# Kernel tuning notes

Hardware: AMD Instinct MI355X
Metric: run time of the kernel (lower is better)

Reference implementation:

```python
import jax, jax.numpy as jnp
import numpy as np

LEVELS = 2
_H0 = jnp.array([0.0322231, -0.01260397, -0.09921954, 0.2978578,
                 0.80373875, 0.49761867, -0.02963553, -0.07576571], dtype=jnp.float32)
_H1 = _H0[::-1] * jnp.array([-1.0, 1.0] * 4, dtype=jnp.float32)  # db4 QMF


def subband_conv2d(x, kernel_2d, stride):
    # depthwise grouped conv: same 2D kernel applied to every channel
    C = x.shape[-1]
    k = jnp.tile(kernel_2d[:, :, None, None], (1, 1, 1, C))  # HWIO with I=1, groups=C
    return jax.lax.conv_general_dilated(
        x, k, window_strides=(stride, stride), padding='SAME',
        dimension_numbers=('NHWC', 'HWIO', 'NHWC'), feature_group_count=C)


def _upsample2d(t):
    B, H, W, C = t.shape
    return jnp.zeros((B, 2 * H, 2 * W, C), t.dtype).at[:, ::2, ::2, :].set(t)


def _local_conv(t, w):
    # per-spatial-position linear map over channels: [B,H,W,I] x [I,O,W,H] -> [B,H,W,O]
    return jnp.einsum('bhwi,iowh->bhwo', t, w)


def setup_inputs() -> dict:
    key = jax.random.key(0)
    ks = jax.random.split(key, 9)
    B, H, W, C, O = 16, 128, 128, 64, 64
    inp = {
        'x': jax.random.normal(ks[0], (B, H, W, C), dtype=jnp.float32),
        'wLL': 0.02 * jax.random.normal(ks[1], (C, O, 32, 32), dtype=jnp.float32),
        'wLH_l0': 0.02 * jax.random.normal(ks[2], (C, O, 64, 64), dtype=jnp.float32),
        'wHL_l0': 0.02 * jax.random.normal(ks[3], (C, O, 64, 64), dtype=jnp.float32),
        'wHH_l0': 0.02 * jax.random.normal(ks[4], (C, O, 64, 64), dtype=jnp.float32),
        'wLH_l1': 0.02 * jax.random.normal(ks[5], (C, O, 32, 32), dtype=jnp.float32),
        'wHL_l1': 0.02 * jax.random.normal(ks[6], (C, O, 32, 32), dtype=jnp.float32),
        'wHH_l1': 0.02 * jax.random.normal(ks[7], (C, O, 32, 32), dtype=jnp.float32),
    }
    return inp


def reference(x, wLL, wLH_l0, wHL_l0, wHH_l0, wLH_l1, wHL_l1, wHH_l1):
    h0, h1 = _H0, _H1
    g0, g1 = h0[::-1], h1[::-1]
    # H=W=128 is divisible by 2**levels, so no symmetric padding is needed.
    res = x
    details = []
    for _ in range(LEVELS):
        cLL = subband_conv2d(res, jnp.outer(h0, h0), 2)
        cLH = subband_conv2d(res, jnp.outer(h0, h1), 2)
        cHL = subband_conv2d(res, jnp.outer(h1, h0), 2)
        cHH = subband_conv2d(res, jnp.outer(h1, h1), 2)
        details.append((cLH, cHL, cHH))
        res = cLL
    yA = _local_conv(res, wLL)  # [B,32,32,O]
    det_w = [(wLH_l0, wHL_l0, wHH_l0), (wLH_l1, wHL_l1, wHH_l1)]
    td = []
    for i in range(LEVELS):
        lh, hl, hh = details[i]
        wlh, whl, whh = det_w[i]
        td.append((_local_conv(lh, wlh), _local_conv(hl, whl), _local_conv(hh, whh)))
    r = yA
    for i in reversed(range(LEVELS)):
        yLH, yHL, yHH = td[i]
        r = (subband_conv2d(_upsample2d(r), jnp.outer(g0, g0), 1)
             + subband_conv2d(_upsample2d(yLH), jnp.outer(g0, g1), 1)
             + subband_conv2d(_upsample2d(yHL), jnp.outer(g1, g0), 1)
             + subband_conv2d(_upsample2d(yHH), jnp.outer(g1, g1), 1))
    return r
```

## Files before the change

### kernel.cpp

```cpp
#include <hip/hip_runtime.h>

__device__ __constant__ float H0[8] = { 0.0322231f, -0.01260397f, -0.09921954f,  0.2978578f,
                                        0.80373875f, 0.49761867f, -0.02963553f, -0.07576571f};
__device__ __constant__ float H1[8] = { 0.07576571f, -0.02963553f, -0.49761867f, 0.80373875f,
                                       -0.2978578f, -0.09921954f,  0.01260397f,  0.0322231f};
__device__ __constant__ float G0[8] = {-0.07576571f, -0.02963553f,  0.49761867f, 0.80373875f,
                                        0.2978578f,  -0.09921954f, -0.01260397f, 0.0322231f};
__device__ __constant__ float G1[8] = { 0.0322231f,   0.01260397f, -0.09921954f, -0.2978578f,
                                        0.80373875f, -0.49761867f, -0.02963553f, 0.07576571f};

template<int HIN>
__global__ __launch_bounds__(256) void fwd_dwt(const float* __restrict__ in,
                                               float* __restrict__ oLL, float* __restrict__ oLH,
                                               float* __restrict__ oHL, float* __restrict__ oHH)
{
    constexpr int OH = HIN / 2;
    constexpr int TQ = OH / 2;
    const int tid = threadIdx.x;
    const int c = tid & 63;
    const int s = blockIdx.x * 4 + (tid >> 6);
    const int j = s % TQ;
    const int i = (s / TQ) % TQ;
    const int b = s / (TQ * TQ);

    float acc[2][2][4];
#pragma unroll
    for (int a = 0; a < 2; ++a)
#pragma unroll
        for (int d = 0; d < 2; ++d)
#pragma unroll
            for (int k = 0; k < 4; ++k) acc[a][d][k] = 0.f;

    const int iw0 = 4 * j - 3;
#pragma unroll
    for (int r = 0; r < 10; ++r) {
        const int ih = 4 * i + r - 3;
        if ((unsigned)ih < (unsigned)HIN) {
            const float* row = in + ((b * HIN + ih) * HIN) * 64 + c;
            float xv[10];
#pragma unroll
            for (int v = 0; v < 10; ++v) {
                const int iw = iw0 + v;
                xv[v] = ((unsigned)iw < (unsigned)HIN) ? row[iw * 64] : 0.f;
            }
            float h00 = 0.f, h01 = 0.f, h10 = 0.f, h11 = 0.f;
#pragma unroll
            for (int v = 0; v < 8; ++v) {
                h00 += H0[v] * xv[v];
                h10 += H1[v] * xv[v];
                h01 += H0[v] * xv[v + 2];
                h11 += H1[v] * xv[v + 2];
            }
#pragma unroll
            for (int ii = 0; ii < 2; ++ii) {
                const int u = r - 2 * ii;
                if (0 <= u && u < 8) {
                    const float a0 = H0[u], a1 = H1[u];
                    acc[ii][0][0] += a0 * h00;
                    acc[ii][0][1] += a0 * h10;
                    acc[ii][0][2] += a1 * h00;
                    acc[ii][0][3] += a1 * h10;
                    acc[ii][1][0] += a0 * h01;
                    acc[ii][1][1] += a0 * h11;
                    acc[ii][1][2] += a1 * h01;
                    acc[ii][1][3] += a1 * h11;
                }
            }
        }
    }

#pragma unroll
    for (int ii = 0; ii < 2; ++ii)
#pragma unroll
        for (int jj = 0; jj < 2; ++jj) {
            const int oh = 2 * i + ii, ow = 2 * j + jj;
            const int oidx = ((b * OH + oh) * OH + ow) * 64 + c;
            oLL[oidx] = acc[ii][jj][0];
            oLH[oidx] = acc[ii][jj][1];
            oHL[oidx] = acc[ii][jj][2];
            oHH[oidx] = acc[ii][jj][3];
        }
}

template<int HD>
__global__ __launch_bounds__(256) void local_conv_lds(
    const float* __restrict__ t0, const float* __restrict__ t1,
    const float* __restrict__ t2, const float* __restrict__ t3,
    const float* __restrict__ w0, const float* __restrict__ w1,
    const float* __restrict__ w2, const float* __restrict__ w3,
    float* __restrict__ o0, float* __restrict__ o1,
    float* __restrict__ o2, float* __restrict__ o3)
{
    constexpr int WH  = HD * HD;
    constexpr int HT  = 16;
    constexpr int RSW = 76;
    constexpr int RSA = 20;

    __shared__ __align__(16) float Wl[4][HT][RSW];
    __shared__ __align__(16) float Al[4][HT][RSA];

    const int z = blockIdx.z;
    const float* tin = (z == 0) ? t0 : (z == 1) ? t1 : (z == 2) ? t2 : t3;
    const float* wgt = (z == 0) ? w0 : (z == 1) ? w1 : (z == 2) ? w2 : w3;
    float*       out = (z == 0) ? o0 : (z == 1) ? o1 : (z == 2) ? o2 : o3;

    const int hbase = blockIdx.x * HT;
    const int w     = blockIdx.y;
    const int tid   = threadIdx.x;

    const int so  = tid >> 2;
    const int sh4 = tid & 3;
    const int sb  = tid >> 4;
    const int sha = tid & 15;

    const int hc = tid & 15;
    const int o4 = tid >> 4;

    const float* wp0 = wgt + (so * WH) + w * HD + hbase + sh4 * 4;
    const float* ap0 = tin + ((sb * HD + hbase + sha) * HD + w) * 64;

    float4 acc[16];
#pragma unroll
    for (int b = 0; b < 16; ++b) acc[b] = make_float4(0.f, 0.f, 0.f, 0.f);

    float4 wv[4], av;
#pragma unroll
    for (int r = 0; r < 4; ++r)
        wv[r] = *(const float4*)(wp0 + (size_t)(r * 64) * WH);
    av = *(const float4*)(ap0);

    for (int chunk = 0; chunk < 16; ++chunk) {
        __syncthreads();
#pragma unroll
        for (int r = 0; r < 4; ++r) {
            Wl[r][sh4 * 4 + 0][so] = wv[r].x;
            Wl[r][sh4 * 4 + 1][so] = wv[r].y;
            Wl[r][sh4 * 4 + 2][so] = wv[r].z;
            Wl[r][sh4 * 4 + 3][so] = wv[r].w;
        }
        Al[0][sha][sb] = av.x;
        Al[1][sha][sb] = av.y;
        Al[2][sha][sb] = av.z;
        Al[3][sha][sb] = av.w;
        __syncthreads();

        if (chunk < 15) {
            const int i0n = (chunk + 1) * 4;
#pragma unroll
            for (int r = 0; r < 4; ++r)
                wv[r] = *(const float4*)(wp0 + (size_t)((i0n + r) * 64) * WH);
            av = *(const float4*)(ap0 + i0n);
        }

#pragma unroll
        for (int ii = 0; ii < 4; ++ii) {
            const float4 wf = *(const float4*)&Wl[ii][hc][o4 * 4];
#pragma unroll
            for (int bq = 0; bq < 4; ++bq) {
                const float4 af = *(const float4*)&Al[ii][hc][bq * 4];
                const float* afp = (const float*)&af;
#pragma unroll
                for (int k = 0; k < 4; ++k) {
                    const float a = afp[k];
                    acc[bq * 4 + k].x += a * wf.x;
                    acc[bq * 4 + k].y += a * wf.y;
                    acc[bq * 4 + k].z += a * wf.z;
                    acc[bq * 4 + k].w += a * wf.w;
                }
            }
        }
    }

#pragma unroll
    for (int b = 0; b < 16; ++b)
        *(float4*)(out + ((b * HD + hbase + hc) * HD + w) * 64 + o4 * 4) = acc[b];
}

template<int HOUT>
__global__ __launch_bounds__(256) void inv_dwt(const float* __restrict__ yLL,
                                               const float* __restrict__ yLH,
                                               const float* __restrict__ yHL,
                                               const float* __restrict__ yHH,
                                               float* __restrict__ out)
{
    constexpr int HS = HOUT / 2;
    const int tid = threadIdx.x;
    const int c = tid & 63;
    const int s = blockIdx.x * 4 + (tid >> 6);
    const int j = s % HS;
    const int i = (s / HS) % HS;
    const int b = s / (HS * HS);

    float Pe[4] = {0.f, 0.f, 0.f, 0.f}, Po[4] = {0.f, 0.f, 0.f, 0.f};
    float Qe[4] = {0.f, 0.f, 0.f, 0.f}, Qo[4] = {0.f, 0.f, 0.f, 0.f};

#pragma unroll
    for (int ku = 0; ku < 4; ++ku) {
        const int m = i - 1 + ku;
        if ((unsigned)m < (unsigned)HS) {
            const float a0e = G0[1 + 2 * ku], a0o = G0[2 * ku];
            const float a1e = G1[1 + 2 * ku], a1o = G1[2 * ku];
            const int rowoff = (b * HS + m) * HS;
#pragma unroll
            for (int kv = 0; kv < 4; ++kv) {
                const int n = j - 1 + kv;
                if ((unsigned)n < (unsigned)HS) {
                    const int idx = (rowoff + n) * 64 + c;
                    const float yll = yLL[idx], ylh = yLH[idx];
                    const float yhl = yHL[idx], yhh = yHH[idx];
                    Pe[kv] += a0e * yll + a1e * yhl;
                    Po[kv] += a0o * yll + a1o * yhl;
                    Qe[kv] += a0e * ylh + a1e * yhh;
                    Qo[kv] += a0o * ylh + a1o * yhh;
                }
            }
        }
    }

    float o00 = 0.f, o01 = 0.f, o10 = 0.f, o11 = 0.f;
#pragma unroll
    for (int kv = 0; kv < 4; ++kv) {
        const float b0e = G0[1 + 2 * kv], b0o = G0[2 * kv];
        const float b1e = G1[1 + 2 * kv], b1o = G1[2 * kv];
        o00 += b0e * Pe[kv] + b1e * Qe[kv];
        o01 += b0o * Pe[kv] + b1o * Qe[kv];
        o10 += b0e * Po[kv] + b1e * Qo[kv];
        o11 += b0o * Po[kv] + b1o * Qo[kv];
    }

    const int h0 = 2 * i, w0 = 2 * j;
    const int base = ((b * HOUT + h0) * HOUT + w0) * 64 + c;
    out[base] = o00;
    out[base + 64] = o01;
    out[base + HOUT * 64] = o10;
    out[base + HOUT * 64 + 64] = o11;
}

extern "C" void kernel_launch(void* const* d_in, const int* in_sizes, int n_in,
                              void* d_out, int out_size, void* d_ws, size_t ws_size,
                              hipStream_t stream)
{
    const float* x    = (const float*)d_in[0];
    const float* wLL  = (const float*)d_in[1];
    const float* wLH0 = (const float*)d_in[2];
    const float* wHL0 = (const float*)d_in[3];
    const float* wHH0 = (const float*)d_in[4];
    const float* wLH1 = (const float*)d_in[5];
    const float* wHL1 = (const float*)d_in[6];
    const float* wHH1 = (const float*)d_in[7];
    float* out = (float*)d_out;
    float* ws  = (float*)d_ws;

    const int S0 = 16 * 64 * 64 * 64;
    const int S1 = 16 * 32 * 32 * 64;

    float* c0LL = out;
    float* c0LH = out + 1 * S0;
    float* c0HL = out + 2 * S0;
    float* c0HH = out + 3 * S0;

    float* c1   = ws;
    float* t0   = ws + 4 * S1;
    float* t1   = ws + 4 * S1 + 3 * S0;
    float* yA   = ws + 7 * S1 + 3 * S0;
    float* r1   = ws;

    fwd_dwt<128><<<16 * 32 * 32 / 4, 256, 0, stream>>>(x, c0LL, c0LH, c0HL, c0HH);

    fwd_dwt<64><<<16 * 16 * 16 / 4, 256, 0, stream>>>(c0LL,
        c1 + 0 * S1, c1 + 1 * S1, c1 + 2 * S1, c1 + 3 * S1);

    local_conv_lds<64><<<dim3(4, 64, 3), 256, 0, stream>>>(
        c0LH, c0HL, c0HH, nullptr,
        wLH0, wHL0, wHH0, nullptr,
        t0 + 0 * S0, t0 + 1 * S0, t0 + 2 * S0, nullptr);

    local_conv_lds<32><<<dim3(2, 32, 4), 256, 0, stream>>>(
        c1 + 1 * S1, c1 + 2 * S1, c1 + 3 * S1, c1 + 0 * S1,
        wLH1, wHL1, wHH1, wLL,
        t1 + 0 * S1, t1 + 1 * S1, t1 + 2 * S1, yA);

    inv_dwt<64><<<16 * 32 * 32 / 4, 256, 0, stream>>>(
        yA, t1 + 0 * S1, t1 + 1 * S1, t1 + 2 * S1, r1);

    inv_dwt<128><<<16 * 64 * 64 / 4, 256, 0, stream>>>(
        r1, t0 + 0 * S0, t0 + 1 * S0, t0 + 2 * S0, out);
}
```

Measured before the change: 291.1 us.

## Retile local conv kernel over output-channel groups and 32-wide h tiles

Restructures the per-position channel-mixing kernel so each block covers 32 spatial h positions and a subset of output channels (OT=16 or 8), instead of 16 positions and all 64 outputs. This raises the block count, especially for the 32x32 level, which before launched few blocks relative to the GPU's CU count. The trade-off is that activations are reloaded once per output-channel group and each thread keeps fewer accumulators, so arithmetic per LDS read drops.

```diff
diff --git a/kernel.cpp b/kernel.cpp
--- a/kernel.cpp
+++ b/kernel.cpp
@@ -82,7 +82,7 @@
         }
 }
 
-template<int HD>
+template<int HD, int OT, int HG>
 __global__ __launch_bounds__(256) void local_conv_lds(
     const float* __restrict__ t0, const float* __restrict__ t1,
     const float* __restrict__ t2, const float* __restrict__ t3,
@@ -92,88 +92,115 @@
     float* __restrict__ o2, float* __restrict__ o3)
 {
     constexpr int WH  = HD * HD;
-    constexpr int HT  = 16;
-    constexpr int RSW = 76;
+    constexpr int NQ  = OT / 4;
+    constexpr int BGN = 8 / NQ;
+    constexpr int BG  = 16 / BGN;
+    constexpr int RSW = OT + 4;
     constexpr int RSA = 20;
-
-    __shared__ __align__(16) float Wl[4][HT][RSW];
-    __shared__ __align__(16) float Al[4][HT][RSA];
+    constexpr int WL4 = OT / 8;
+
+    __shared__ __align__(16) float Wl[4][32][RSW];
+    __shared__ __align__(16) float Al[4][32][RSA];
 
     const int z = blockIdx.z;
     const float* tin = (z == 0) ? t0 : (z == 1) ? t1 : (z == 2) ? t2 : t3;
     const float* wgt = (z == 0) ? w0 : (z == 1) ? w1 : (z == 2) ? w2 : w3;
     float*       out = (z == 0) ? o0 : (z == 1) ? o1 : (z == 2) ? o2 : o3;
 
-    const int hbase = blockIdx.x * HT;
+    const int bx    = blockIdx.x;
+    const int hg    = bx % HG;
+    const int og    = bx / HG;
+    const int hbase = hg * 32;
     const int w     = blockIdx.y;
-    const int tid   = threadIdx.x;
-
-    const int so  = tid >> 2;
-    const int sh4 = tid & 3;
-    const int sb  = tid >> 4;
-    const int sha = tid & 15;
-
-    const int hc = tid & 15;
-    const int o4 = tid >> 4;
-
-    const float* wp0 = wgt + (so * WH) + w * HD + hbase + sh4 * 4;
-    const float* ap0 = tin + ((sb * HD + hbase + sha) * HD + w) * 64;
-
-    float4 acc[16];
-#pragma unroll
-    for (int b = 0; b < 16; ++b) acc[b] = make_float4(0.f, 0.f, 0.f, 0.f);
-
-    float4 wv[4], av;
-#pragma unroll
-    for (int r = 0; r < 4; ++r)
-        wv[r] = *(const float4*)(wp0 + (size_t)(r * 64) * WH);
-    av = *(const float4*)(ap0);
+    const int t     = threadIdx.x;
+
+    int whq[WL4], wo[WL4], wi[WL4];
+#pragma unroll
+    for (int l = 0; l < WL4; ++l) {
+        const int idx = t + 256 * l;
+        whq[l] = idx & 7;
+        wo[l]  = (idx >> 3) & (OT - 1);
+        wi[l]  = idx >> (3 + (OT == 16 ? 4 : 3));
+    }
+    const int ah0 = t & 31, ab0 = t >> 5;
+
+    const int hc = t & 31;
+    const int r  = t >> 5;
+    const int oq = r & (NQ - 1);
+    const int bg = r / NQ;
+
+    float4 acc4[BG];
+#pragma unroll
+    for (int j = 0; j < BG; ++j) acc4[j] = make_float4(0.f, 0.f, 0.f, 0.f);
+
+    float4 wv[WL4], av[2];
+#pragma unroll
+    for (int l = 0; l < WL4; ++l)
+        wv[l] = *(const float4*)(wgt + (size_t)(wi[l] * 64 + og * OT + wo[l]) * WH
+                                 + w * HD + hbase + whq[l] * 4);
+#pragma unroll
+    for (int l = 0; l < 2; ++l) {
+        const int b = ab0 + 8 * l;
+        av[l] = *(const float4*)(tin + (size_t)((b * HD + hbase + ah0) * HD + w) * 64);
+    }
 
     for (int chunk = 0; chunk < 16; ++chunk) {
         __syncthreads();
 #pragma unroll
-        for (int r = 0; r < 4; ++r) {
-            Wl[r][sh4 * 4 + 0][so] = wv[r].x;
-            Wl[r][sh4 * 4 + 1][so] = wv[r].y;
-            Wl[r][sh4 * 4 + 2][so] = wv[r].z;
-            Wl[r][sh4 * 4 + 3][so] = wv[r].w;
-        }
-        Al[0][sha][sb] = av.x;
-        Al[1][sha][sb] = av.y;
-        Al[2][sha][sb] = av.z;
-        Al[3][sha][sb] = av.w;
+        for (int l = 0; l < WL4; ++l) {
+            Wl[wi[l]][whq[l] * 4 + 0][wo[l]] = wv[l].x;
+            Wl[wi[l]][whq[l] * 4 + 1][wo[l]] = wv[l].y;
+            Wl[wi[l]][whq[l] * 4 + 2][wo[l]] = wv[l].z;
+            Wl[wi[l]][whq[l] * 4 + 3][wo[l]] = wv[l].w;
+        }
+#pragma unroll
+        for (int l = 0; l < 2; ++l) {
+            const int b = ab0 + 8 * l;
+            Al[0][ah0][b] = av[l].x;
+            Al[1][ah0][b] = av[l].y;
+            Al[2][ah0][b] = av[l].z;
+            Al[3][ah0][b] = av[l].w;
+        }
         __syncthreads();
 
         if (chunk < 15) {
             const int i0n = (chunk + 1) * 4;
 #pragma unroll
-            for (int r = 0; r < 4; ++r)
-                wv[r] = *(const float4*)(wp0 + (size_t)((i0n + r) * 64) * WH);
-            av = *(const float4*)(ap0 + i0n);
+            for (int l = 0; l < WL4; ++l)
+                wv[l] = *(const float4*)(wgt + (size_t)((i0n + wi[l]) * 64 + og * OT + wo[l]) * WH
+                                         + w * HD + hbase + whq[l] * 4);
+#pragma unroll
+            for (int l = 0; l < 2; ++l) {
+                const int b = ab0 + 8 * l;
+                av[l] = *(const float4*)(tin + (size_t)((b * HD + hbase + ah0) * HD + w) * 64 + i0n);
+            }
         }
 
 #pragma unroll
         for (int ii = 0; ii < 4; ++ii) {
-            const float4 wf = *(const float4*)&Wl[ii][hc][o4 * 4];
-#pragma unroll
-            for (int bq = 0; bq < 4; ++bq) {
-                const float4 af = *(const float4*)&Al[ii][hc][bq * 4];
+            const float4 wf = *(const float4*)&Wl[ii][hc][oq * 4];
+#pragma unroll
+            for (int bb = 0; bb < BG / 4; ++bb) {
+                const float4 af = *(const float4*)&Al[ii][hc][bg * BG + bb * 4];
                 const float* afp = (const float*)&af;
 #pragma unroll
                 for (int k = 0; k < 4; ++k) {
                     const float a = afp[k];
-                    acc[bq * 4 + k].x += a * wf.x;
-                    acc[bq * 4 + k].y += a * wf.y;
-                    acc[bq * 4 + k].z += a * wf.z;
-                    acc[bq * 4 + k].w += a * wf.w;
+                    acc4[bb * 4 + k].x += a * wf.x;
+                    acc4[bb * 4 + k].y += a * wf.y;
+                    acc4[bb * 4 + k].z += a * wf.z;
+                    acc4[bb * 4 + k].w += a * wf.w;
                 }
             }
         }
     }
 
-#pragma unroll
-    for (int b = 0; b < 16; ++b)
-        *(float4*)(out + ((b * HD + hbase + hc) * HD + w) * 64 + o4 * 4) = acc[b];
+    const int obase = og * OT + oq * 4;
+#pragma unroll
+    for (int j = 0; j < BG; ++j) {
+        const int b = bg * BG + j;
+        *(float4*)(out + (size_t)((b * HD + hbase + hc) * HD + w) * 64 + obase) = acc4[j];
+    }
 }
 
 template<int HOUT>
@@ -270,12 +297,12 @@
     fwd_dwt<64><<<16 * 16 * 16 / 4, 256, 0, stream>>>(c0LL,
         c1 + 0 * S1, c1 + 1 * S1, c1 + 2 * S1, c1 + 3 * S1);
 
-    local_conv_lds<64><<<dim3(4, 64, 3), 256, 0, stream>>>(
+    local_conv_lds<64, 16, 2><<<dim3(8, 64, 3), 256, 0, stream>>>(
         c0LH, c0HL, c0HH, nullptr,
         wLH0, wHL0, wHH0, nullptr,
         t0 + 0 * S0, t0 + 1 * S0, t0 + 2 * S0, nullptr);
 
-    local_conv_lds<32><<<dim3(2, 32, 4), 256, 0, stream>>>(
+    local_conv_lds<32, 8, 1><<<dim3(8, 32, 4), 256, 0, stream>>>(
         c1 + 1 * S1, c1 + 2 * S1, c1 + 3 * S1, c1 + 0 * S1,
         wLH1, wHL1, wHH1, wLL,
         t1 + 0 * S1, t1 + 1 * S1, t1 + 2 * S1, yA);
```

Result: slower. 518.3 us (+78.1%).
